# Performance work log

Measured on AMD Instinct MI355X. Metric: run time of the kernel, lower is better.

The kernel has to match this reference:

```python
import jax, jax.numpy as jnp
import numpy as np

N = 1024   # nodes
E = 65536  # edges per relation
H = 2      # attention heads
NEG_SLOPE = 0.2


def _add_self_loops(ei, n):
    loop = jnp.arange(n, dtype=ei.dtype)
    return jnp.concatenate([ei, jnp.stack([loop, loop])], axis=1)


def _gat(x, ei, W, a_src, a_dst, bias, n):
    # PyG GATConv (heads=H, concat=True): project, edge attention, segment softmax, scatter-sum
    h, c = a_src.shape
    xp = (x @ W).reshape(n, h, c)                      # [n, H, C]
    src, dst = ei[0], ei[1]
    al_s = jnp.einsum('nhc,hc->nh', xp, a_src)         # [n, H]
    al_d = jnp.einsum('nhc,hc->nh', xp, a_dst)
    alpha = jax.nn.leaky_relu(al_s[src] + al_d[dst], NEG_SLOPE)  # [E, H]
    m = jax.ops.segment_max(alpha, dst, num_segments=n)
    m = jnp.where(jnp.isfinite(m), m, 0.0)
    m = jax.lax.stop_gradient(m)
    e = jnp.exp(alpha - m[dst])
    s = jax.ops.segment_sum(e, dst, num_segments=n)
    a = e / (s[dst] + 1e-16)                           # segment softmax over incoming edges
    out = jax.ops.segment_sum(xp[src] * a[:, :, None], dst, num_segments=n)
    return out.reshape(n, h * c) + bias


def setup_inputs():
    key = jax.random.key(0)
    ks = jax.random.split(key, 32)
    d = {}
    d['x'] = jax.random.normal(ks[0], (N, 256), dtype=jnp.float32)
    d['ei0'] = jax.random.randint(ks[1], (2, E), 0, N)
    d['ei1'] = jax.random.randint(ks[2], (2, E), 0, N)
    k = 3
    # layer 1: in 256 -> H*256 = 512 per relation
    for r in range(2):
        d[f'W1_{r}'] = jax.random.normal(ks[k], (256, H * 256), jnp.float32) * 0.0625; k += 1
        d[f'as1_{r}'] = jax.random.normal(ks[k], (H, 256), jnp.float32) * 0.0625; k += 1
        d[f'ad1_{r}'] = jax.random.normal(ks[k], (H, 256), jnp.float32) * 0.0625; k += 1
        d[f'b1_{r}'] = jnp.zeros((H * 256,), jnp.float32)
    # layer 2: in 512 -> H*64 = 128 per relation
    for r in range(2):
        d[f'W2_{r}'] = jax.random.normal(ks[k], (512, H * 64), jnp.float32) * 0.0442; k += 1
        d[f'as2_{r}'] = jax.random.normal(ks[k], (H, 64), jnp.float32) * 0.125; k += 1
        d[f'ad2_{r}'] = jax.random.normal(ks[k], (H, 64), jnp.float32) * 0.125; k += 1
        d[f'b2_{r}'] = jnp.zeros((H * 64,), jnp.float32)
    d['w_lin'] = jax.random.normal(ks[k], (H * 64, 1), jnp.float32) * 0.088; k += 1
    d['b_lin'] = jnp.zeros((1,), jnp.float32)
    return d


def reference(x, ei0, ei1, W1_0, as1_0, ad1_0, b1_0, W1_1, as1_1, ad1_1, b1_1,
              W2_0, as2_0, ad2_0, b2_0, W2_1, as2_1, ad2_1, b2_1, w_lin, b_lin):
    e0 = _add_self_loops(ei0, N)
    e1 = _add_self_loops(ei1, N)
    # HeteroConv aggr='sum' over the two relations
    h1 = _gat(x, e0, W1_0, as1_0, ad1_0, b1_0, N) + _gat(x, e1, W1_1, as1_1, ad1_1, b1_1, N)
    h1 = jax.nn.relu(h1)
    h2 = _gat(h1, e0, W2_0, as2_0, ad2_0, b2_0, N) + _gat(h1, e1, W2_1, as2_1, ad2_1, b2_1, N)
    # dense pairwise sum over all node pairs: [N*N, 128]
    pairs = (h2[:, None, :] + h2[None, :, :]).reshape(N * N, h2.shape[-1])
    return pairs @ w_lin + b_lin
```

## Files before the change

### kernel.cpp

```cpp
#include <hip/hip_runtime.h>
#include <hip/hip_bf16.h>


#define NEG_SLOPE 0.2f
static __device__ __forceinline__ float lrelu(float x){ return x > 0.f ? x : NEG_SLOPE * x; }

#define NN 1024
#define SLOTS 192

static __device__ __forceinline__ int norm_cnt(int raw){
    return raw < -1000000000 ? raw - (int)0xAAAAAAAAu : raw;
}

struct P {
    const float *x; const int *ei0, *ei1;
    const float *W1_0,*as1_0,*ad1_0,*b1_0, *W1_1,*as1_1,*ad1_1,*b1_1;
    const float *W2_0,*as2_0,*ad2_0,*b2_0, *W2_1,*as2_1,*ad2_1,*b2_1;
    const float *wlin, *blin;
    float *out;
    __hip_bfloat162 *xp1_0,*xp1_1;
    float *L1;
    float *wc;
    float *nb;
    float *q, *qb;
    int *cnt;
    unsigned short *eb;
    int E;
};

__global__ __launch_bounds__(256)
void k1_scatter_gemm1(P p){
    __shared__ float As[32][68];
    __shared__ float Bs[32][68];
    const int b = blockIdx.x, t = threadIdx.x;

    if (b < 128){
        const int TOT = p.E + NN;
        for (int i = b*256 + t; i < 2*TOT; i += 128*256){
            int r = i >= TOT, e = i - r*TOT;
            const int* ei = r ? p.ei1 : p.ei0;
            int src, dst;
            if (e < p.E){ src = ei[e]; dst = ei[p.E + e]; } else { src = dst = e - p.E; }
            int pos = norm_cnt(atomicAdd(&p.cnt[r*NN + dst], 1));
            if (pos >= 0 && pos < SLOTS)
                p.eb[(dst*2 + r)*SLOTS + pos] = (unsigned short)src;
        }
        return;
    }
    if (b >= 384){
        int idx2 = b - 384;
        int r = idx2 >> 2, k0 = (idx2 & 3) * 128;
        const float* W2 = r ? p.W2_1 : p.W2_0;
        const float* as2 = r ? p.as2_1 : p.as2_0;
        const float* ad2 = r ? p.ad2_1 : p.ad2_0;
        if (t < 128){
            int k = k0 + t;
            const float* row = W2 + k*128;
            float sa[2] = {0.f,0.f}, da[2] = {0.f,0.f}, za[2] = {0.f,0.f};
            #pragma unroll
            for (int h = 0; h < 2; h++){
                #pragma unroll
                for (int c4 = 0; c4 < 16; c4++){
                    float4 w  = *(const float4*)(row + h*64 + c4*4);
                    float4 av = *(const float4*)(as2 + h*64 + c4*4);
                    float4 dv = *(const float4*)(ad2 + h*64 + c4*4);
                    float4 zv = *(const float4*)(p.wlin + h*64 + c4*4);
                    sa[h] += w.x*av.x + w.y*av.y + w.z*av.z + w.w*av.w;
                    da[h] += w.x*dv.x + w.y*dv.y + w.z*dv.z + w.w*dv.w;
                    za[h] += w.x*zv.x + w.y*zv.y + w.z*zv.z + w.w*zv.w;
                }
            }
            float* wcr = p.wc + r*6*512;
            wcr[0*512 + k] = sa[0]; wcr[1*512 + k] = sa[1];
            wcr[2*512 + k] = da[0]; wcr[3*512 + k] = da[1];
            wcr[4*512 + k] = za[0]; wcr[5*512 + k] = za[1];
        }
        if (b == 384 && t == 128){
            float s = 0.f;
            for (int k = 0; k < 128; k++) s += (p.b2_0[k] + p.b2_1[k]) * p.wlin[k];
            p.qb[0] = s;
        }
        return;
    }
    int idx = b - 128;
    int r = idx >> 7, t2 = idx & 127;
    int m0 = (t2 >> 3) * 64, n0 = (t2 & 7) * 64;
    const float* B = r ? p.W1_1 : p.W1_0;
    __hip_bfloat162* C = r ? p.xp1_1 : p.xp1_0;
    int tx = t & 15, ty = t >> 4;
    const int am0 = t >> 3,  ac40 = t & 7;
    const int am1 = (256+t) >> 3, ac41 = t & 7;
    const int bk0 = t >> 4,  bc40 = t & 15;
    const int bk1 = (256+t) >> 4, bc41 = t & 15;
    float acc[4][4] = {};
    float4 a4[2], b4[2];
    a4[0] = *(const float4*)(p.x + (size_t)(m0+am0)*256 + 0 + ac40*4);
    a4[1] = *(const float4*)(p.x + (size_t)(m0+am1)*256 + 0 + ac41*4);
    b4[0] = *(const float4*)(B + (size_t)(0+bk0)*512 + n0 + bc40*4);
    b4[1] = *(const float4*)(B + (size_t)(0+bk1)*512 + n0 + bc41*4);
    for (int k0 = 0; k0 < 256; k0 += 32){
        __syncthreads();
        As[ac40*4+0][am0] = a4[0].x; As[ac40*4+1][am0] = a4[0].y;
        As[ac40*4+2][am0] = a4[0].z; As[ac40*4+3][am0] = a4[0].w;
        As[ac41*4+0][am1] = a4[1].x; As[ac41*4+1][am1] = a4[1].y;
        As[ac41*4+2][am1] = a4[1].z; As[ac41*4+3][am1] = a4[1].w;
        *(float4*)&Bs[bk0][bc40*4] = b4[0];
        *(float4*)&Bs[bk1][bc41*4] = b4[1];
        __syncthreads();
        if (k0 + 32 < 256){
            int kn = k0 + 32;
            a4[0] = *(const float4*)(p.x + (size_t)(m0+am0)*256 + kn + ac40*4);
            a4[1] = *(const float4*)(p.x + (size_t)(m0+am1)*256 + kn + ac41*4);
            b4[0] = *(const float4*)(B + (size_t)(kn+bk0)*512 + n0 + bc40*4);
            b4[1] = *(const float4*)(B + (size_t)(kn+bk1)*512 + n0 + bc41*4);
        }
        #pragma unroll
        for (int kk = 0; kk < 32; kk++){
            float4 av = *(const float4*)&As[kk][ty*4];
            float4 bv = *(const float4*)&Bs[kk][tx*4];
            float ar[4] = {av.x, av.y, av.z, av.w};
            float br[4] = {bv.x, bv.y, bv.z, bv.w};
            #pragma unroll
            for (int i = 0; i < 4; i++)
                #pragma unroll
                for (int j = 0; j < 4; j++)
                    acc[i][j] += ar[i] * br[j];
        }
    }
    #pragma unroll
    for (int i = 0; i < 4; i++){
        int row = m0 + ty*4 + i, col = n0 + tx*4;
        __hip_bfloat162 t0, t1;
        t0.x = __float2bfloat16(acc[i][0]); t0.y = __float2bfloat16(acc[i][1]);
        t1.x = __float2bfloat16(acc[i][2]); t1.y = __float2bfloat16(acc[i][3]);
        size_t o2 = ((size_t)row*512 + col) >> 1;
        C[o2] = t0; C[o2 + 1] = t1;
    }
    {
        int h = n0 >> 8;
        const float* as_ = r ? p.as1_1 : p.as1_0;
        const float* ad_ = r ? p.ad1_1 : p.ad1_0;
        float a_s[4], a_d[4];
        #pragma unroll
        for (int u = 0; u < 4; u++){
            a_s[u] = as_[n0 + tx*4 + u];
            a_d[u] = ad_[n0 + tx*4 + u];
        }
        #pragma unroll
        for (int i = 0; i < 4; i++){
            float ps = acc[i][0]*a_s[0] + acc[i][1]*a_s[1]
                     + acc[i][2]*a_s[2] + acc[i][3]*a_s[3];
            float pd = acc[i][0]*a_d[0] + acc[i][1]*a_d[1]
                     + acc[i][2]*a_d[2] + acc[i][3]*a_d[3];
            #pragma unroll
            for (int o = 8; o > 0; o >>= 1){
                ps += __shfl_down(ps, o, 16);
                pd += __shfl_down(pd, o, 16);
            }
            if (tx == 0){
                int row = m0 + ty*4 + i;
                atomicAdd(&p.L1[row*8 + r*4 + h],     ps);
                atomicAdd(&p.L1[row*8 + r*4 + 2 + h], pd);
            }
        }
    }
}

__global__ __launch_bounds__(256)
void k2_agg1(P p){
    __shared__ float wa0[2][SLOTS], wa1[2][SLOTS];
    __shared__ int   ssrc[2][SLOTS];
    __shared__ float rsum[4][2];
    __shared__ float invs[2][2];
    __shared__ float pacc[4][64][8];
    const int v = blockIdx.x, t = threadIdx.x;
    const int par = t >> 6;
    const int c16 = t & 63;
    const bool head0 = c16 < 32;

    const int r1 = t >> 7, slot1 = t & 127;
    int endv[2];
    endv[0] = min(norm_cnt(p.cnt[v]),      SLOTS);
    endv[1] = min(norm_cnt(p.cnt[NN + v]), SLOTS);
    int sA = p.eb[(v*2 + r1)*SLOTS + slot1];
    const bool xact = (par == 0) || (par == 2);
    const int r2x = (par == 2) ? 1 : 0;
    const int slot2 = 128 + (t & 63);
    int sB = p.eb[(v*2 + r2x)*SLOTS + slot2];
    float2 ldv0 = *(const float2*)(p.L1 + v*8 + 0*4 + 2);
    float2 ldv1 = *(const float2*)(p.L1 + v*8 + 1*4 + 2);
    float2 ldA = r1  ? ldv1 : ldv0;
    float2 ldB = r2x ? ldv1 : ldv0;
    float2 lsA = *(const float2*)(p.L1 + sA*8 + r1*4);
    float2 lsB = *(const float2*)(p.L1 + sB*8 + r2x*4);
    bool actA = slot1 < endv[r1];
    bool actB = xact && (slot2 < endv[r2x]);
    float e0 = actA ? __expf(lrelu(lsA.x + ldA.x)) : 0.f;
    float e1 = actA ? __expf(lrelu(lsA.y + ldA.y)) : 0.f;
    float f0 = actB ? __expf(lrelu(lsB.x + ldB.x)) : 0.f;
    float f1 = actB ? __expf(lrelu(lsB.y + ldB.y)) : 0.f;
    if (actA){ wa0[r1][slot1] = e0; wa1[r1][slot1] = e1; ssrc[r1][slot1] = sA*256; }
    if (actB){ wa0[r2x][slot2] = f0; wa1[r2x][slot2] = f1; ssrc[r2x][slot2] = sB*256; }
    float s0 = e0 + f0, s1 = e1 + f1;
    #pragma unroll
    for (int o = 32; o > 0; o >>= 1){
        s0 += __shfl_down(s0, o, 64);
        s1 += __shfl_down(s1, o, 64);
    }
    if (c16 == 0){ rsum[par][0] = s0; rsum[par][1] = s1; }
    __syncthreads();
    if (t == 0){
        invs[0][0] = 1.f / (rsum[0][0] + rsum[1][0] + 1e-16f);
        invs[0][1] = 1.f / (rsum[0][1] + rsum[1][1] + 1e-16f);
        invs[1][0] = 1.f / (rsum[2][0] + rsum[3][0] + 1e-16f);
        invs[1][1] = 1.f / (rsum[2][1] + rsum[3][1] + 1e-16f);
    }
    __syncthreads();

    float acc[8] = {};
    #pragma unroll
    for (int r = 0; r < 2; r++){
        const __hip_bfloat162* xp = r ? p.xp1_1 : p.xp1_0;
        const int end = endv[r];
        const float inv = head0 ? invs[r][0] : invs[r][1];
        #pragma unroll 4
        for (int i = par; i < end; i += 4){
            const __hip_bfloat162* rp = xp + ssrc[r][i] + c16*4;
            float4 raw = *(const float4*)rp;
            const __hip_bfloat162* w = (const __hip_bfloat162*)&raw;
            float a = (head0 ? wa0[r][i] : wa1[r][i]) * inv;
            #pragma unroll
            for (int u = 0; u < 4; u++){
                acc[2*u+0] += __bfloat162float(w[u].x) * a;
                acc[2*u+1] += __bfloat162float(w[u].y) * a;
            }
        }
    }
    __syncthreads();
    #pragma unroll
    for (int u = 0; u < 8; u++) pacc[par][c16][u] = acc[u];
    __syncthreads();

    {
        int cb = c16 * 8;
        float o[8];
        #pragma unroll
        for (int u = 0; u < 8; u++){
            float s = pacc[0][c16][u] + pacc[1][c16][u]
                    + pacc[2][c16][u] + pacc[3][c16][u];
            s += p.b1_0[cb+u] + p.b1_1[cb+u];
            o[u] = s > 0.f ? s : 0.f;
        }
        const int slot[6] = {0, 1, 4, 5, 2, 3};
        #pragma unroll
        for (int k = 0; k < 3; k++){
            int idx = par*3 + k;
            int r2 = idx / 6, j = idx % 6;
            const float* w = p.wc + ((r2*6 + j) << 9) + cb;
            float s = o[0]*w[0] + o[1]*w[1] + o[2]*w[2] + o[3]*w[3]
                    + o[4]*w[4] + o[5]*w[5] + o[6]*w[6] + o[7]*w[7];
            #pragma unroll
            for (int off = 32; off > 0; off >>= 1) s += __shfl_down(s, off, 64);
            if (c16 == 0) p.nb[(v*2 + r2)*8 + slot[j]] = s;
        }
    }
}

__global__ __launch_bounds__(256)
void k3_agg2(P p){
    __shared__ float red[2][2][4];
    const int b = blockIdx.x, t = threadIdx.x, lane = t & 63, wave = t >> 6;
    const int nl = wave >> 1, r = wave & 1;
    const int v = b*2 + nl;
    const unsigned short* eb = p.eb + (v*2 + r)*SLOTS;
    int s_pre = eb[lane];
    int end = min(norm_cnt(p.cnt[r*NN + v]), SLOTS);
    const float* nbv = p.nb + (v*2 + r)*8;
    float ld0 = nbv[4], ld1 = nbv[5];
    float4 g0 = *(const float4*)(p.nb + (s_pre*2 + r)*8);
    bool act = lane < end;
    float e0 = act ? __expf(lrelu(g0.x + ld0)) : 0.f;
    float e1 = act ? __expf(lrelu(g0.y + ld1)) : 0.f;
    float d0 = e0, d1 = e1;
    float n0 = act ? e0 * g0.z : 0.f;
    float n1 = act ? e1 * g0.w : 0.f;
    for (int e = lane + 64; e < end; e += 64){
        int s = eb[e];
        float4 g = *(const float4*)(p.nb + (s*2 + r)*8);
        float a0 = __expf(lrelu(g.x + ld0));
        float a1 = __expf(lrelu(g.y + ld1));
        d0 += a0; d1 += a1;
        n0 += a0 * g.z; n1 += a1 * g.w;
    }
    #pragma unroll
    for (int o = 1; o < 64; o <<= 1){
        d0 += __shfl_xor(d0, o, 64); d1 += __shfl_xor(d1, o, 64);
        n0 += __shfl_xor(n0, o, 64); n1 += __shfl_xor(n1, o, 64);
    }
    if (lane == 0){
        red[nl][r][0] = d0; red[nl][r][1] = d1;
        red[nl][r][2] = n0; red[nl][r][3] = n1;
    }
    __syncthreads();
    if (t == nl*128){
        float qv = p.qb[0];
        #pragma unroll
        for (int rr = 0; rr < 2; rr++){
            qv += red[nl][rr][2] / (red[nl][rr][0] + 1e-16f);
            qv += red[nl][rr][3] / (red[nl][rr][1] + 1e-16f);
        }
        p.q[v] = qv;
    }
}

__global__ __launch_bounds__(256)
void k4_pairs(P p){
    const int b = blockIdx.x, t = threadIdx.x;
    float4 qj = ((const float4*)p.q)[t];
    float bl = p.blin[0];
    #pragma unroll
    for (int ii = 0; ii < 4; ++ii){
        int i = b*4 + ii;
        float qi = p.q[i] + bl;
        float4 o = { qi + qj.x, qi + qj.y, qi + qj.z, qi + qj.w };
        ((float4*)p.out)[(size_t)i * 256 + t] = o;
    }
}

extern "C" void kernel_launch(void* const* d_in, const int* in_sizes, int n_in,
                              void* d_out, int out_size, void* d_ws, size_t ws_size,
                              hipStream_t stream){
    P prm;
    prm.x    = (const float*)d_in[0];
    prm.ei0  = (const int*)d_in[1];
    prm.ei1  = (const int*)d_in[2];
    prm.W1_0 = (const float*)d_in[3];  prm.as1_0 = (const float*)d_in[4];
    prm.ad1_0 = (const float*)d_in[5]; prm.b1_0  = (const float*)d_in[6];
    prm.W1_1 = (const float*)d_in[7];  prm.as1_1 = (const float*)d_in[8];
    prm.ad1_1 = (const float*)d_in[9]; prm.b1_1  = (const float*)d_in[10];
    prm.W2_0 = (const float*)d_in[11]; prm.as2_0 = (const float*)d_in[12];
    prm.ad2_0 = (const float*)d_in[13]; prm.b2_0 = (const float*)d_in[14];
    prm.W2_1 = (const float*)d_in[15]; prm.as2_1 = (const float*)d_in[16];
    prm.ad2_1 = (const float*)d_in[17]; prm.b2_1 = (const float*)d_in[18];
    prm.wlin = (const float*)d_in[19];
    prm.blin = (const float*)d_in[20];
    prm.out  = (float*)d_out;
    prm.E    = in_sizes[1] / 2;
    const int N = NN;

    char* wp = (char*)d_ws;
    auto alloc = [&](size_t bytes) -> char* {
        char* r = wp; wp += (bytes + 255) & ~(size_t)255; return r;
    };
    prm.xp1_0 = (__hip_bfloat162*)alloc((size_t)N*512*2);
    prm.xp1_1 = (__hip_bfloat162*)alloc((size_t)N*512*2);
    prm.cnt = (int*)alloc((size_t)2*N*4);
    prm.L1  = (float*)alloc((size_t)N*8*4);
    prm.wc  = (float*)alloc((size_t)2*6*512*4);
    prm.nb  = (float*)alloc((size_t)N*2*8*4);
    prm.eb  = (unsigned short*)alloc((size_t)N*2*SLOTS*2);
    prm.q   = (float*)alloc(N*4);
    prm.qb  = (float*)alloc(256);

    k1_scatter_gemm1<<<392, 256, 0, stream>>>(prm);
    k2_agg1<<<NN, 256, 0, stream>>>(prm);
    k3_agg2<<<NN/2, 256, 0, stream>>>(prm);
    k4_pairs<<<NN/4, 256, 0, stream>>>(prm);
}
```

Measured before the change: 145.9 us.

## Fuse layer-2 aggregation into pairwise output kernel with redundant per-block compute

Merges the layer-2 attention aggregation and the dense pairwise output into a single kernel. Every block loads the per-node attention table into shared memory and recomputes all node scores itself, one thread per node-relation, before writing its slice of output rows. This removes one kernel launch and the global round trip of the score vector. The cost is fully redundant aggregation work in every block, with serial per-thread edge loops and uncoalesced edge-list reads.

```diff
diff --git a/kernel.cpp b/kernel.cpp
--- a/kernel.cpp
+++ b/kernel.cpp
@@ -22,7 +22,7 @@
     float *L1;
     float *wc;
     float *nb;
-    float *q, *qb;
+    float *qb;
     int *cnt;
     unsigned short *eb;
     int E;
@@ -267,62 +267,59 @@
 }
 
 __global__ __launch_bounds__(256)
-void k3_agg2(P p){
-    __shared__ float red[2][2][4];
-    const int b = blockIdx.x, t = threadIdx.x, lane = t & 63, wave = t >> 6;
-    const int nl = wave >> 1, r = wave & 1;
-    const int v = b*2 + nl;
-    const unsigned short* eb = p.eb + (v*2 + r)*SLOTS;
-    int s_pre = eb[lane];
-    int end = min(norm_cnt(p.cnt[r*NN + v]), SLOTS);
-    const float* nbv = p.nb + (v*2 + r)*8;
-    float ld0 = nbv[4], ld1 = nbv[5];
-    float4 g0 = *(const float4*)(p.nb + (s_pre*2 + r)*8);
-    bool act = lane < end;
-    float e0 = act ? __expf(lrelu(g0.x + ld0)) : 0.f;
-    float e1 = act ? __expf(lrelu(g0.y + ld1)) : 0.f;
-    float d0 = e0, d1 = e1;
-    float n0 = act ? e0 * g0.z : 0.f;
-    float n1 = act ? e1 * g0.w : 0.f;
-    for (int e = lane + 64; e < end; e += 64){
-        int s = eb[e];
-        float4 g = *(const float4*)(p.nb + (s*2 + r)*8);
-        float a0 = __expf(lrelu(g.x + ld0));
-        float a1 = __expf(lrelu(g.y + ld1));
-        d0 += a0; d1 += a1;
-        n0 += a0 * g.z; n1 += a1 * g.w;
-    }
-    #pragma unroll
-    for (int o = 1; o < 64; o <<= 1){
-        d0 += __shfl_xor(d0, o, 64); d1 += __shfl_xor(d1, o, 64);
-        n0 += __shfl_xor(n0, o, 64); n1 += __shfl_xor(n1, o, 64);
-    }
-    if (lane == 0){
-        red[nl][r][0] = d0; red[nl][r][1] = d1;
-        red[nl][r][2] = n0; red[nl][r][3] = n1;
-    }
-    __syncthreads();
-    if (t == nl*128){
-        float qv = p.qb[0];
-        #pragma unroll
-        for (int rr = 0; rr < 2; rr++){
-            qv += red[nl][rr][2] / (red[nl][rr][0] + 1e-16f);
-            qv += red[nl][rr][3] / (red[nl][rr][1] + 1e-16f);
-        }
-        p.q[v] = qv;
-    }
-}
-
-__global__ __launch_bounds__(256)
-void k4_pairs(P p){
+void k3_agg2_pairs(P p){
+    __shared__ float4 lnb[2048];
+    __shared__ float qc[2048];
+    __shared__ float A[1024];
     const int b = blockIdx.x, t = threadIdx.x;
-    float4 qj = ((const float4*)p.q)[t];
+
+    float2 ldp[8]; int endv[8];
+    #pragma unroll
+    for (int k = 0; k < 8; k++){
+        int nr = t + (k << 8);
+        lnb[nr]  = *(const float4*)(p.nb + nr*8);
+        ldp[k]   = *(const float2*)(p.nb + nr*8 + 4);
+        int v = nr >> 1, r = nr & 1;
+        endv[k] = min(norm_cnt(p.cnt[r*NN + v]), SLOTS);
+    }
+    __syncthreads();
+
+    #pragma unroll
+    for (int k = 0; k < 8; k++){
+        int nr = t + (k << 8);
+        int r = nr & 1;
+        const unsigned short* ebp = p.eb + nr*SLOTS;
+        float ld0 = ldp[k].x, ld1 = ldp[k].y;
+        float d0 = 0.f, d1 = 0.f, n0 = 0.f, n1 = 0.f;
+        int end = endv[k];
+        #pragma unroll 4
+        for (int e = 0; e < end; e++){
+            int s = ebp[e];
+            float4 g = lnb[(s << 1) + r];
+            float e0 = __expf(lrelu(g.x + ld0));
+            float e1 = __expf(lrelu(g.y + ld1));
+            d0 += e0; d1 += e1;
+            n0 += e0 * g.z; n1 += e1 * g.w;
+        }
+        qc[nr] = n0/(d0 + 1e-16f) + n1/(d1 + 1e-16f);
+    }
+    __syncthreads();
+
+    float qb0 = p.qb[0];
+    #pragma unroll
+    for (int k = 0; k < 4; k++){
+        int j = t + (k << 8);
+        A[j] = qb0 + qc[2*j] + qc[2*j + 1];
+    }
+    __syncthreads();
+
     float bl = p.blin[0];
-    #pragma unroll
-    for (int ii = 0; ii < 4; ++ii){
-        int i = b*4 + ii;
-        float qi = p.q[i] + bl;
-        float4 o = { qi + qj.x, qi + qj.y, qi + qj.z, qi + qj.w };
+    float4 aj = ((const float4*)A)[t];
+    #pragma unroll
+    for (int ii = 0; ii < 4; ii++){
+        int i = (b << 2) + ii;
+        float qi = A[i] + bl;
+        float4 o = { qi + aj.x, qi + aj.y, qi + aj.z, qi + aj.w };
         ((float4*)p.out)[(size_t)i * 256 + t] = o;
     }
 }
@@ -359,11 +356,9 @@
     prm.wc  = (float*)alloc((size_t)2*6*512*4);
     prm.nb  = (float*)alloc((size_t)N*2*8*4);
     prm.eb  = (unsigned short*)alloc((size_t)N*2*SLOTS*2);
-    prm.q   = (float*)alloc(N*4);
     prm.qb  = (float*)alloc(256);
 
     k1_scatter_gemm1<<<392, 256, 0, stream>>>(prm);
     k2_agg1<<<NN, 256, 0, stream>>>(prm);
-    k3_agg2<<<NN/2, 256, 0, stream>>>(prm);
-    k4_pairs<<<NN/4, 256, 0, stream>>>(prm);
-}
+    k3_agg2_pairs<<<NN/4, 256, 0, stream>>>(prm);
+}
```

Result: slower. 202.1 us (+38.4%).
